# Kernel tuning notes

Measured on AMD Instinct MI355X. Metric: run time of the kernel, lower is better.

The kernel has to match this reference:

```python
import jax, jax.numpy as jnp
import numpy as np
import math

DIM = 1024
HEADS = 16
B, N = 2, 2048

POLY = jnp.array([-0.037, 0.481, -2.3, 4.917, -1.791], dtype=jnp.float32)


def adaptive_temperature_softmax(logits):
    # logits: [b, h, n, n]
    original_probs = jax.nn.softmax(logits, axis=-1)
    entropy = jnp.sum(-original_probs * jnp.log(original_probs + 1e-9), axis=-1, keepdims=True)
    e2 = entropy * entropy
    poly_result = POLY[0] * e2 * e2 + POLY[1] * e2 * entropy + POLY[2] * e2 + POLY[3] * entropy + POLY[4]
    beta = jnp.where(entropy > 0.5, jnp.maximum(poly_result, 1.0), 1.0)
    return jax.nn.softmax(logits * beta, axis=-1)


def setup_inputs() -> dict:
    key = jax.random.key(0)
    ks = jax.random.split(key, 5)
    s = 1.0 / math.sqrt(DIM)
    return {
        "x": jax.random.normal(ks[0], (B, N, DIM), dtype=jnp.float32),
        "Wq": jax.random.normal(ks[1], (DIM, DIM), dtype=jnp.float32) * s,
        "Wk": jax.random.normal(ks[2], (DIM, DIM), dtype=jnp.float32) * s,
        "Wv": jax.random.normal(ks[3], (DIM, DIM), dtype=jnp.float32) * s,
        "Wo": jax.random.normal(ks[4], (DIM, DIM), dtype=jnp.float32) * s,
        "bo": jnp.zeros((DIM,), dtype=jnp.float32),
    }


def reference(x, Wq, Wk, Wv, Wo, bo):
    b, n, d = x.shape
    h = HEADS
    hd = d // h
    # torch nn.Linear: y = x @ W.T (+ bias)
    def proj(W):
        t = x @ W.T  # [b, n, d]
        return t.reshape(b, n, h, hd).transpose(0, 2, 1, 3)  # [b, h, n, hd]
    q, k, v = proj(Wq), proj(Wk), proj(Wv)
    sim = jnp.einsum('bhid,bhjd->bhij', q, k) / math.sqrt(hd)
    neg = -jnp.finfo(sim.dtype).max
    causal = jnp.triu(jnp.ones((n, n), dtype=bool), k=1)  # True above diagonal
    sim = jnp.where(causal, neg, sim)
    attn = adaptive_temperature_softmax(sim)
    out = jnp.einsum('bhij,bhjd->bhid', attn, v)
    out = out.transpose(0, 2, 1, 3).reshape(b, n, d)
    return out @ Wo.T + bo
```

## Files before the change

### kernel.cpp

```cpp
#include <hip/hip_runtime.h>
#include <math.h>

#define B_   2
#define N_   2048
#define D_   1024
#define H_   16
#define HD_  64
#define BH_  32
#define M_   4096

typedef __bf16 bf16x8 __attribute__((ext_vector_type(8)));
typedef float  f32x4  __attribute__((ext_vector_type(4)));

__device__ inline unsigned short f2b(float f) {
    unsigned u = __float_as_uint(f);
    u += 0x7FFFu + ((u >> 16) & 1u);
    return (unsigned short)(u >> 16);
}
__device__ inline unsigned short f2b_fast(float f) {
    return (unsigned short)((__float_as_uint(f) + 0x8000u) >> 16);
}

__global__ __launch_bounds__(256)
void cvt_all(const float* __restrict__ x,  const float* __restrict__ wq,
             const float* __restrict__ wk, const float* __restrict__ wv,
             const float* __restrict__ wo, ushort* __restrict__ dst)
{
    int i = blockIdx.x * 256 + threadIdx.x;
    if (i >= 2097152) return;
    int fi = i * 4;
    const float* s; int off;
    if (fi < 4194304) { s = x; off = fi; }
    else {
        int r = fi - 4194304;
        int wsel = r >> 20;
        off = r & 1048575;
        s = (wsel == 0) ? wq : (wsel == 1) ? wk : (wsel == 2) ? wv : wo;
    }
    float4 f = *(const float4*)(s + off);
    ushort4 o;
    o.x = f2b(f.x); o.y = f2b(f.y); o.z = f2b(f.z); o.w = f2b(f.w);
    *(ushort4*)(dst + fi) = o;
}

__global__ __launch_bounds__(256)
void gemm_qkv(const ushort* __restrict__ A,
              const ushort* __restrict__ W0, const ushort* __restrict__ W1,
              const ushort* __restrict__ W2,
              ushort* __restrict__ O0, ushort* __restrict__ O1,
              ushort* __restrict__ O2)
{
    const int z = blockIdx.z;
    const ushort* W = (z == 0) ? W0 : (z == 1) ? W1 : W2;

    __shared__ alignas(16) ushort As[128][40];
    __shared__ alignas(16) ushort Bs[128][40];

    const int t = threadIdx.x;
    const int lane = t & 63, w = t >> 6;
    const int quad = lane >> 4, l15 = lane & 15;
    const int wm = (w >> 1) * 64, wn = (w & 1) * 64;
    const int tileM = blockIdx.x * 128, tileN = blockIdx.y * 128;

    const int r0 = t >> 2, r1 = 64 + (t >> 2);
    const int cg = (t & 3) * 8;
    const ushort* GA0 = A + (size_t)(tileM + r0) * D_ + cg;
    const ushort* GA1 = A + (size_t)(tileM + r1) * D_ + cg;
    const ushort* GB0 = W + (size_t)(tileN + r0) * D_ + cg;
    const ushort* GB1 = W + (size_t)(tileN + r1) * D_ + cg;

    f32x4 acc[4][4];
#pragma unroll
    for (int mt = 0; mt < 4; ++mt)
#pragma unroll
        for (int nt = 0; nt < 4; ++nt) acc[mt][nt] = (f32x4){0.f, 0.f, 0.f, 0.f};

    uint4 pa0 = *(const uint4*)GA0, pa1 = *(const uint4*)GA1;
    uint4 pb0 = *(const uint4*)GB0, pb1 = *(const uint4*)GB1;

    for (int k0 = 0; k0 < D_; k0 += 32) {
        __syncthreads();
        *(uint4*)&As[r0][cg] = pa0;
        *(uint4*)&As[r1][cg] = pa1;
        *(uint4*)&Bs[r0][cg] = pb0;
        *(uint4*)&Bs[r1][cg] = pb1;
        __syncthreads();
        if (k0 + 32 < D_) {
            pa0 = *(const uint4*)(GA0 + k0 + 32);
            pa1 = *(const uint4*)(GA1 + k0 + 32);
            pb0 = *(const uint4*)(GB0 + k0 + 32);
            pb1 = *(const uint4*)(GB1 + k0 + 32);
        }

        bf16x8 af[4], bf[4];
#pragma unroll
        for (int mt = 0; mt < 4; ++mt) af[mt] = *(const bf16x8*)&As[wm + mt * 16 + l15][quad * 8];
#pragma unroll
        for (int nt = 0; nt < 4; ++nt) bf[nt] = *(const bf16x8*)&Bs[wn + nt * 16 + l15][quad * 8];
#pragma unroll
        for (int mt = 0; mt < 4; ++mt)
#pragma unroll
            for (int nt = 0; nt < 4; ++nt)
                acc[mt][nt] = __builtin_amdgcn_mfma_f32_16x16x32_bf16(af[mt], bf[nt], acc[mt][nt], 0, 0, 0);
    }

    ushort* O = (z == 0) ? O0 : (z == 1) ? O1 : O2;
    const float scl = (z == 0) ? 0.18033688f : 1.0f;
#pragma unroll
    for (int mt = 0; mt < 4; ++mt)
#pragma unroll
        for (int nt = 0; nt < 4; ++nt) {
            if (z == 2) {
                int rg0 = tileM + wm + mt * 16 + quad * 4;
                int cgc = tileN + wn + nt * 16 + l15;
                int b = rg0 >> 11, n0 = rg0 & (N_ - 1);
                int h = cgc >> 6, dd = cgc & 63;
                ushort4 o4;
                o4.x = f2b(acc[mt][nt][0]); o4.y = f2b(acc[mt][nt][1]);
                o4.z = f2b(acc[mt][nt][2]); o4.w = f2b(acc[mt][nt][3]);
                *(ushort4*)&O[((size_t)((b * H_ + h) * HD_ + dd)) * N_ + n0] = o4;
            } else {
#pragma unroll
                for (int r = 0; r < 4; ++r) {
                    int rg = tileM + wm + mt * 16 + quad * 4 + r;
                    int cgc = tileN + wn + nt * 16 + l15;
                    int b = rg >> 11, n = rg & (N_ - 1);
                    int h = cgc >> 6, dd = cgc & 63;
                    O[(((size_t)(b * H_ + h)) * N_ + n) * HD_ + dd] = f2b(acc[mt][nt][r] * scl);
                }
            }
        }
}

__global__ __launch_bounds__(256)
void gemm_fin(const ushort* __restrict__ A, const ushort* __restrict__ W,
              const float* __restrict__ bias, float* __restrict__ Of)
{
    __shared__ alignas(16) ushort As[128][40];
    __shared__ alignas(16) ushort Bs[64][40];

    const int t = threadIdx.x;
    const int lane = t & 63, w = t >> 6;
    const int quad = lane >> 4, l15 = lane & 15;
    const int wm = (w >> 1) * 64, wn = (w & 1) * 32;
    const int tileM = blockIdx.x * 128, tileN = blockIdx.y * 64;

    const int r0 = t >> 2, r1 = 64 + (t >> 2);
    const int cg = (t & 3) * 8;
    const ushort* GA0 = A + (size_t)(tileM + r0) * D_ + cg;
    const ushort* GA1 = A + (size_t)(tileM + r1) * D_ + cg;
    const ushort* GB0 = W + (size_t)(tileN + r0) * D_ + cg;

    f32x4 acc[4][2];
#pragma unroll
    for (int mt = 0; mt < 4; ++mt)
#pragma unroll
        for (int nt = 0; nt < 2; ++nt) acc[mt][nt] = (f32x4){0.f, 0.f, 0.f, 0.f};

    uint4 pa0 = *(const uint4*)GA0, pa1 = *(const uint4*)GA1;
    uint4 pb0 = *(const uint4*)GB0;

    for (int k0 = 0; k0 < D_; k0 += 32) {
        __syncthreads();
        *(uint4*)&As[r0][cg] = pa0;
        *(uint4*)&As[r1][cg] = pa1;
        *(uint4*)&Bs[r0 & 63][cg] = pb0;
        __syncthreads();
        if (k0 + 32 < D_) {
            pa0 = *(const uint4*)(GA0 + k0 + 32);
            pa1 = *(const uint4*)(GA1 + k0 + 32);
            pb0 = *(const uint4*)(GB0 + k0 + 32);
        }

        bf16x8 af[4], bf[2];
#pragma unroll
        for (int mt = 0; mt < 4; ++mt) af[mt] = *(const bf16x8*)&As[wm + mt * 16 + l15][quad * 8];
#pragma unroll
        for (int nt = 0; nt < 2; ++nt) bf[nt] = *(const bf16x8*)&Bs[wn + nt * 16 + l15][quad * 8];
#pragma unroll
        for (int mt = 0; mt < 4; ++mt)
#pragma unroll
            for (int nt = 0; nt < 2; ++nt)
                acc[mt][nt] = __builtin_amdgcn_mfma_f32_16x16x32_bf16(af[mt], bf[nt], acc[mt][nt], 0, 0, 0);
    }

#pragma unroll
    for (int mt = 0; mt < 4; ++mt)
#pragma unroll
        for (int nt = 0; nt < 2; ++nt)
#pragma unroll
            for (int r = 0; r < 4; ++r) {
                int rg = tileM + wm + mt * 16 + quad * 4 + r;
                int cgc = tileN + wn + nt * 16 + l15;
                Of[(size_t)rg * D_ + cgc] = acc[mt][nt][r] + bias[cgc];
            }
}

__global__ __launch_bounds__(256)
void attn_mfma(const ushort* __restrict__ Q, const ushort* __restrict__ K,
               const ushort* __restrict__ VT, ushort* __restrict__ AO)
{
    const int bid = blockIdx.x;
    const int qt = 31 - (bid >> 5);
    const int bh = bid & 31;
    const size_t kvbase = (size_t)bh * N_ * HD_;

    __shared__ alignas(16) ushort Ks[128][72];
    __shared__ alignas(16) ushort Vs[64][136];
    __shared__ alignas(16) ushort Ps[4][4][296];

    const int t = threadIdx.x;
    const int lane = t & 63, w = t >> 6;
    const int quad = lane >> 4, l15 = lane & 15;
    const float SH2 = 11.5416913f;
    const float LN2 = 0.69314718f;

    const int skey = t >> 3;
    const int skc  = (t & 7) * 8;
    const ushort* KS = K + kvbase + (size_t)skey * HD_ + skc;
    const int vhd = t >> 4;
    const int vkc = (t & 15) * 8;
    const ushort* VS = VT + kvbase + (size_t)vhd * N_ + vkc;

    const int qrow = w * 16 + quad * 4;
    const int qglob = qt * 64 + qrow;
    const int b = bh >> 4, h = bh & 15;
    const int nCh = (qt + 2) >> 1;

    bf16x8 aq0, aq1;
    {
        const size_t qr = kvbase + (size_t)(qt * 64 + w * 16 + l15) * HD_;
        aq0 = *(const bf16x8*)&Q[qr + quad * 8];
        aq1 = *(const bf16x8*)&Q[qr + 32 + quad * 8];
    }

    float ez[4] = {0.f, 0.f, 0.f, 0.f};
    float sz[4] = {0.f, 0.f, 0.f, 0.f};

    uint4 k0 = *(const uint4*)KS;
    uint4 k1 = *(const uint4*)(KS + 32 * HD_);
    uint4 k2 = *(const uint4*)(KS + 64 * HD_);
    uint4 k3 = *(const uint4*)(KS + 96 * HD_);
    for (int c = 0; c < nCh; ++c) {
        __syncthreads();
        *(uint4*)&Ks[skey][skc]      = k0;
        *(uint4*)&Ks[32 + skey][skc] = k1;
        *(uint4*)&Ks[64 + skey][skc] = k2;
        *(uint4*)&Ks[96 + skey][skc] = k3;
        __syncthreads();
        if (c + 1 < nCh) {
            const ushort* nb = KS + (size_t)(c + 1) * (128 * HD_);
            k0 = *(const uint4*)nb;
            k1 = *(const uint4*)(nb + 32 * HD_);
            k2 = *(const uint4*)(nb + 64 * HD_);
            k3 = *(const uint4*)(nb + 96 * HD_);
        }
        if (c + 1 < nCh) {
#pragma unroll
            for (int nt = 0; nt < 8; ++nt) {
                f32x4 sv = (f32x4){0.f, 0.f, 0.f, 0.f};
                sv = __builtin_amdgcn_mfma_f32_16x16x32_bf16(aq0, *(const bf16x8*)&Ks[nt * 16 + l15][quad * 8], sv, 0, 0, 0);
                sv = __builtin_amdgcn_mfma_f32_16x16x32_bf16(aq1, *(const bf16x8*)&Ks[nt * 16 + l15][32 + quad * 8], sv, 0, 0, 0);
#pragma unroll
                for (int r = 0; r < 4; ++r) {
                    float sh = sv[r] - SH2;
                    float e = __builtin_amdgcn_exp2f(sh);
                    ez[r] += e;
                    sz[r] = fmaf(e, sh, sz[r]);
                }
            }
        } else {
            const int tiles = (((qt + 1) * 64) - c * 128) >> 4;
            const int kb0 = c * 128;
            for (int nt = 0; nt < tiles; ++nt) {
                f32x4 sv = (f32x4){0.f, 0.f, 0.f, 0.f};
                sv = __builtin_amdgcn_mfma_f32_16x16x32_bf16(aq0, *(const bf16x8*)&Ks[nt * 16 + l15][quad * 8], sv, 0, 0, 0);
                sv = __builtin_amdgcn_mfma_f32_16x16x32_bf16(aq1, *(const bf16x8*)&Ks[nt * 16 + l15][32 + quad * 8], sv, 0, 0, 0);
                const int kcol = kb0 + nt * 16 + l15;
#pragma unroll
                for (int r = 0; r < 4; ++r) {
                    float sh = sv[r] - SH2;
                    float e = (kcol <= qglob + r) ? __builtin_amdgcn_exp2f(sh) : 0.f;
                    ez[r] += e;
                    sz[r] = fmaf(e, sh, sz[r]);
                }
            }
        }
    }
#pragma unroll
    for (int r = 0; r < 4; ++r) {
#pragma unroll
        for (int off = 1; off < 16; off <<= 1) {
            ez[r] += __shfl_xor(ez[r], off);
            sz[r] += __shfl_xor(sz[r], off);
        }
    }

    float nbs[4], bl[4];
#pragma unroll
    for (int r = 0; r < 4; ++r) {
        float Z = ez[r];
        float Hh = LN2 * (__builtin_amdgcn_logf(Z) - sz[r] / Z);
        float bb = 1.f;
        if (Hh > 0.5f) {
            float e2 = Hh * Hh;
            float pp = -0.037f * e2 * e2 + 0.481f * e2 * Hh - 2.3f * e2 + 4.917f * Hh - 1.791f;
            bb = fmaxf(pp, 1.f);
        }
        bl[r] = bb;
        nbs[r] = -bb * SH2;
    }

    f32x4 ov[4];
#pragma unroll
    for (int nt = 0; nt < 4; ++nt) ov[nt] = (f32x4){0.f, 0.f, 0.f, 0.f};
    float zp[4] = {0.f, 0.f, 0.f, 0.f};

    k0 = *(const uint4*)KS;
    k1 = *(const uint4*)(KS + 32 * HD_);
    k2 = *(const uint4*)(KS + 64 * HD_);
    k3 = *(const uint4*)(KS + 96 * HD_);
    uint4 v0 = *(const uint4*)VS;
    uint4 v1 = *(const uint4*)(VS + 16 * N_);
    uint4 v2 = *(const uint4*)(VS + 32 * N_);
    uint4 v3 = *(const uint4*)(VS + 48 * N_);
    for (int c = 0; c < nCh; ++c) {
        __syncthreads();
        *(uint4*)&Ks[skey][skc]      = k0;
        *(uint4*)&Ks[32 + skey][skc] = k1;
        *(uint4*)&Ks[64 + skey][skc] = k2;
        *(uint4*)&Ks[96 + skey][skc] = k3;
        *(uint4*)&Vs[vhd][vkc]       = v0;
        *(uint4*)&Vs[16 + vhd][vkc]  = v1;
        *(uint4*)&Vs[32 + vhd][vkc]  = v2;
        *(uint4*)&Vs[48 + vhd][vkc]  = v3;
        __syncthreads();
        if (c + 1 < nCh) {
            const ushort* nk = KS + (size_t)(c + 1) * (128 * HD_);
            k0 = *(const uint4*)nk;
            k1 = *(const uint4*)(nk + 32 * HD_);
            k2 = *(const uint4*)(nk + 64 * HD_);
            k3 = *(const uint4*)(nk + 96 * HD_);
            const ushort* nv = VS + (c + 1) * 128;
            v0 = *(const uint4*)nv;
            v1 = *(const uint4*)(nv + 16 * N_);
            v2 = *(const uint4*)(nv + 32 * N_);
            v3 = *(const uint4*)(nv + 48 * N_);
        }
        const int halves = min(2, (qt + 1) - c * 2);
        for (int hh = 0; hh < halves; ++hh) {
            const bool diag = (c * 2 + hh == qt);

            float wv[4][4];
#pragma unroll
            for (int nt = 0; nt < 4; ++nt) {
                f32x4 sv = (f32x4){0.f, 0.f, 0.f, 0.f};
                sv = __builtin_amdgcn_mfma_f32_16x16x32_bf16(aq0, *(const bf16x8*)&Ks[hh * 64 + nt * 16 + l15][quad * 8], sv, 0, 0, 0);
                sv = __builtin_amdgcn_mfma_f32_16x16x32_bf16(aq1, *(const bf16x8*)&Ks[hh * 64 + nt * 16 + l15][32 + quad * 8], sv, 0, 0, 0);
                const int kcol = nt * 16 + l15;
#pragma unroll
                for (int r = 0; r < 4; ++r) {
                    float e = __builtin_amdgcn_exp2f(fmaf(bl[r], sv[r], nbs[r]));
                    wv[nt][r] = (!diag || (kcol <= qrow + r)) ? e : 0.f;
                }
            }
#pragma unroll
            for (int nt = 0; nt < 4; ++nt)
#pragma unroll
                for (int r = 0; r < 4; ++r)
                    Ps[w][quad][r * 72 + nt * 16 + l15] = f2b_fast(wv[nt][r]);
#pragma unroll
            for (int r = 0; r < 4; ++r)
                zp[r] += (wv[0][r] + wv[1][r]) + (wv[2][r] + wv[3][r]);

            bf16x8 pa0 = *(const bf16x8*)&Ps[w][l15 >> 2][(l15 & 3) * 72 + quad * 8];
            bf16x8 pa1 = *(const bf16x8*)&Ps[w][l15 >> 2][(l15 & 3) * 72 + 32 + quad * 8];
#pragma unroll
            for (int nt = 0; nt < 4; ++nt) {
                ov[nt] = __builtin_amdgcn_mfma_f32_16x16x32_bf16(pa0, *(const bf16x8*)&Vs[nt * 16 + l15][hh * 64 + quad * 8], ov[nt], 0, 0, 0);
                ov[nt] = __builtin_amdgcn_mfma_f32_16x16x32_bf16(pa1, *(const bf16x8*)&Vs[nt * 16 + l15][hh * 64 + 32 + quad * 8], ov[nt], 0, 0, 0);
            }
        }
    }
#pragma unroll
    for (int r = 0; r < 4; ++r)
#pragma unroll
        for (int off = 1; off < 16; off <<= 1) zp[r] += __shfl_xor(zp[r], off);

#pragma unroll
    for (int r = 0; r < 4; ++r) {
        int qg = qt * 64 + w * 16 + quad * 4 + r;
        float inv = 1.f / zp[r];
        size_t rowoff = ((size_t)(b * N_ + qg)) * D_ + h * HD_;
#pragma unroll
        for (int nt = 0; nt < 4; ++nt)
            AO[rowoff + nt * 16 + l15] = f2b(ov[nt][r] * inv);
    }
}

extern "C" void kernel_launch(void* const* d_in, const int* in_sizes, int n_in,
                              void* d_out, int out_size, void* d_ws, size_t ws_size,
                              hipStream_t stream)
{
    const float* x  = (const float*)d_in[0];
    const float* Wq = (const float*)d_in[1];
    const float* Wk = (const float*)d_in[2];
    const float* Wv = (const float*)d_in[3];
    const float* Wo = (const float*)d_in[4];
    const float* bo = (const float*)d_in[5];
    float* out = (float*)d_out;

    ushort* ws  = (ushort*)d_ws;
    ushort* xb  = ws;
    ushort* wqb = ws + 4194304;
    ushort* wkb = ws + 5242880;
    ushort* wvb = ws + 6291456;
    ushort* wob = ws + 7340032;
    ushort* Qb  = ws + 8388608;
    ushort* Kb  = ws + 12582912;
    ushort* Vtb = ws + 16777216;
    ushort* aob = ws + 20971520;

    cvt_all<<<8192, 256, 0, stream>>>(x, Wq, Wk, Wv, Wo, xb);

    gemm_qkv<<<dim3(32, 8, 3), 256, 0, stream>>>(
        xb, wqb, wkb, wvb, Qb, Kb, Vtb);

    attn_mfma<<<dim3(1024), 256, 0, stream>>>(Qb, Kb, Vtb, aob);

    gemm_fin<<<dim3(32, 16), 256, 0, stream>>>(aob, wob, bo, out);
}
```

Baseline: 202.2 us.

## Process two 64-row query tiles per attention block to reuse K/V loads

Each attention block now handles a 128-row query tile as two 64-row sub-tiles (A and B) that share every K and V chunk loaded into shared memory, and the grid is halved to 512 blocks. The aim is to halve global and shared-memory traffic for K/V and amortise the barriers over twice the MFMA work. The cost is more registers per thread (two sets of Q fragments, accumulators and statistics), which may lower occupancy. Fewer, heavier blocks may also leave compute units less evenly loaded under the causal work imbalance.

```diff
diff --git a/kernel.cpp b/kernel.cpp
--- a/kernel.cpp
+++ b/kernel.cpp
@@ -201,7 +201,7 @@
                const ushort* __restrict__ VT, ushort* __restrict__ AO)
 {
     const int bid = blockIdx.x;
-    const int qt = 31 - (bid >> 5);
+    const int qtt = 15 - (bid >> 5);
     const int bh = bid & 31;
     const size_t kvbase = (size_t)bh * N_ * HD_;
 
@@ -222,20 +222,21 @@
     const int vkc = (t & 15) * 8;
     const ushort* VS = VT + kvbase + (size_t)vhd * N_ + vkc;
 
-    const int qrow = w * 16 + quad * 4;
-    const int qglob = qt * 64 + qrow;
+    const int qrowL = w * 16 + quad * 4;
     const int b = bh >> 4, h = bh & 15;
-    const int nCh = (qt + 2) >> 1;
-
-    bf16x8 aq0, aq1;
+    const int nCh = qtt + 1;
+
+    bf16x8 aq0A, aq1A, aq0B, aq1B;
     {
-        const size_t qr = kvbase + (size_t)(qt * 64 + w * 16 + l15) * HD_;
-        aq0 = *(const bf16x8*)&Q[qr + quad * 8];
-        aq1 = *(const bf16x8*)&Q[qr + 32 + quad * 8];
-    }
-
-    float ez[4] = {0.f, 0.f, 0.f, 0.f};
-    float sz[4] = {0.f, 0.f, 0.f, 0.f};
+        const size_t qrA = kvbase + (size_t)(qtt * 128 + w * 16 + l15) * HD_;
+        aq0A = *(const bf16x8*)&Q[qrA + quad * 8];
+        aq1A = *(const bf16x8*)&Q[qrA + 32 + quad * 8];
+        aq0B = *(const bf16x8*)&Q[qrA + 64 * HD_ + quad * 8];
+        aq1B = *(const bf16x8*)&Q[qrA + 64 * HD_ + 32 + quad * 8];
+    }
+
+    float ezA[4] = {0.f, 0.f, 0.f, 0.f}, szA[4] = {0.f, 0.f, 0.f, 0.f};
+    float ezB[4] = {0.f, 0.f, 0.f, 0.f}, szB[4] = {0.f, 0.f, 0.f, 0.f};
 
     uint4 k0 = *(const uint4*)KS;
     uint4 k1 = *(const uint4*)(KS + 32 * HD_);
@@ -255,34 +256,60 @@
             k2 = *(const uint4*)(nb + 64 * HD_);
             k3 = *(const uint4*)(nb + 96 * HD_);
         }
-        if (c + 1 < nCh) {
+        if (c < qtt) {
 #pragma unroll
             for (int nt = 0; nt < 8; ++nt) {
-                f32x4 sv = (f32x4){0.f, 0.f, 0.f, 0.f};
-                sv = __builtin_amdgcn_mfma_f32_16x16x32_bf16(aq0, *(const bf16x8*)&Ks[nt * 16 + l15][quad * 8], sv, 0, 0, 0);
-                sv = __builtin_amdgcn_mfma_f32_16x16x32_bf16(aq1, *(const bf16x8*)&Ks[nt * 16 + l15][32 + quad * 8], sv, 0, 0, 0);
+                bf16x8 kf0 = *(const bf16x8*)&Ks[nt * 16 + l15][quad * 8];
+                bf16x8 kf1 = *(const bf16x8*)&Ks[nt * 16 + l15][32 + quad * 8];
+                f32x4 svA = (f32x4){0.f, 0.f, 0.f, 0.f};
+                svA = __builtin_amdgcn_mfma_f32_16x16x32_bf16(aq0A, kf0, svA, 0, 0, 0);
+                svA = __builtin_amdgcn_mfma_f32_16x16x32_bf16(aq1A, kf1, svA, 0, 0, 0);
+                f32x4 svB = (f32x4){0.f, 0.f, 0.f, 0.f};
+                svB = __builtin_amdgcn_mfma_f32_16x16x32_bf16(aq0B, kf0, svB, 0, 0, 0);
+                svB = __builtin_amdgcn_mfma_f32_16x16x32_bf16(aq1B, kf1, svB, 0, 0, 0);
 #pragma unroll
                 for (int r = 0; r < 4; ++r) {
-                    float sh = sv[r] - SH2;
-                    float e = __builtin_amdgcn_exp2f(sh);
-                    ez[r] += e;
-                    sz[r] = fmaf(e, sh, sz[r]);
+                    float shA = svA[r] - SH2, shB = svB[r] - SH2;
+                    float eA = __builtin_amdgcn_exp2f(shA);
+                    float eB = __builtin_amdgcn_exp2f(shB);
+                    ezA[r] += eA; szA[r] = fmaf(eA, shA, szA[r]);
+                    ezB[r] += eB; szB[r] = fmaf(eB, shB, szB[r]);
                 }
             }
         } else {
-            const int tiles = (((qt + 1) * 64) - c * 128) >> 4;
-            const int kb0 = c * 128;
-            for (int nt = 0; nt < tiles; ++nt) {
-                f32x4 sv = (f32x4){0.f, 0.f, 0.f, 0.f};
-                sv = __builtin_amdgcn_mfma_f32_16x16x32_bf16(aq0, *(const bf16x8*)&Ks[nt * 16 + l15][quad * 8], sv, 0, 0, 0);
-                sv = __builtin_amdgcn_mfma_f32_16x16x32_bf16(aq1, *(const bf16x8*)&Ks[nt * 16 + l15][32 + quad * 8], sv, 0, 0, 0);
-                const int kcol = kb0 + nt * 16 + l15;
+#pragma unroll
+            for (int nt = 0; nt < 4; ++nt) {
+                bf16x8 kf0 = *(const bf16x8*)&Ks[nt * 16 + l15][quad * 8];
+                bf16x8 kf1 = *(const bf16x8*)&Ks[nt * 16 + l15][32 + quad * 8];
+                f32x4 svA = (f32x4){0.f, 0.f, 0.f, 0.f};
+                svA = __builtin_amdgcn_mfma_f32_16x16x32_bf16(aq0A, kf0, svA, 0, 0, 0);
+                svA = __builtin_amdgcn_mfma_f32_16x16x32_bf16(aq1A, kf1, svA, 0, 0, 0);
+                f32x4 svB = (f32x4){0.f, 0.f, 0.f, 0.f};
+                svB = __builtin_amdgcn_mfma_f32_16x16x32_bf16(aq0B, kf0, svB, 0, 0, 0);
+                svB = __builtin_amdgcn_mfma_f32_16x16x32_bf16(aq1B, kf1, svB, 0, 0, 0);
+                const int kcol = nt * 16 + l15;
 #pragma unroll
                 for (int r = 0; r < 4; ++r) {
-                    float sh = sv[r] - SH2;
-                    float e = (kcol <= qglob + r) ? __builtin_amdgcn_exp2f(sh) : 0.f;
-                    ez[r] += e;
-                    sz[r] = fmaf(e, sh, sz[r]);
+                    float shA = svA[r] - SH2, shB = svB[r] - SH2;
+                    float eA = (kcol <= qrowL + r) ? __builtin_amdgcn_exp2f(shA) : 0.f;
+                    float eB = __builtin_amdgcn_exp2f(shB);
+                    ezA[r] += eA; szA[r] = fmaf(eA, shA, szA[r]);
+                    ezB[r] += eB; szB[r] = fmaf(eB, shB, szB[r]);
+                }
+            }
+#pragma unroll
+            for (int nt = 4; nt < 8; ++nt) {
+                bf16x8 kf0 = *(const bf16x8*)&Ks[nt * 16 + l15][quad * 8];
+                bf16x8 kf1 = *(const bf16x8*)&Ks[nt * 16 + l15][32 + quad * 8];
+                f32x4 svB = (f32x4){0.f, 0.f, 0.f, 0.f};
+                svB = __builtin_amdgcn_mfma_f32_16x16x32_bf16(aq0B, kf0, svB, 0, 0, 0);
+                svB = __builtin_amdgcn_mfma_f32_16x16x32_bf16(aq1B, kf1, svB, 0, 0, 0);
+                const int kcol = (nt - 4) * 16 + l15;
+#pragma unroll
+                for (int r = 0; r < 4; ++r) {
+                    float shB = svB[r] - SH2;
+                    float eB = (kcol <= qrowL + r) ? __builtin_amdgcn_exp2f(shB) : 0.f;
+                    ezB[r] += eB; szB[r] = fmaf(eB, shB, szB[r]);
                 }
             }
         }
@@ -291,30 +318,43 @@
     for (int r = 0; r < 4; ++r) {
 #pragma unroll
         for (int off = 1; off < 16; off <<= 1) {
-            ez[r] += __shfl_xor(ez[r], off);
-            sz[r] += __shfl_xor(sz[r], off);
-        }
-    }
-
-    float nbs[4], bl[4];
+            ezA[r] += __shfl_xor(ezA[r], off);
+            szA[r] += __shfl_xor(szA[r], off);
+            ezB[r] += __shfl_xor(ezB[r], off);
+            szB[r] += __shfl_xor(szB[r], off);
+        }
+    }
+
+    float nbsA[4], blA[4], nbsB[4], blB[4];
 #pragma unroll
     for (int r = 0; r < 4; ++r) {
-        float Z = ez[r];
-        float Hh = LN2 * (__builtin_amdgcn_logf(Z) - sz[r] / Z);
+        float Z = ezA[r];
+        float Hh = LN2 * (__builtin_amdgcn_logf(Z) - szA[r] / Z);
         float bb = 1.f;
         if (Hh > 0.5f) {
             float e2 = Hh * Hh;
             float pp = -0.037f * e2 * e2 + 0.481f * e2 * Hh - 2.3f * e2 + 4.917f * Hh - 1.791f;
             bb = fmaxf(pp, 1.f);
         }
-        bl[r] = bb;
-        nbs[r] = -bb * SH2;
-    }
-
-    f32x4 ov[4];
-#pragma unroll
-    for (int nt = 0; nt < 4; ++nt) ov[nt] = (f32x4){0.f, 0.f, 0.f, 0.f};
-    float zp[4] = {0.f, 0.f, 0.f, 0.f};
+        blA[r] = bb; nbsA[r] = -bb * SH2;
+        Z = ezB[r];
+        Hh = LN2 * (__builtin_amdgcn_logf(Z) - szB[r] / Z);
+        bb = 1.f;
+        if (Hh > 0.5f) {
+            float e2 = Hh * Hh;
+            float pp = -0.037f * e2 * e2 + 0.481f * e2 * Hh - 2.3f * e2 + 4.917f * Hh - 1.791f;
+            bb = fmaxf(pp, 1.f);
+        }
+        blB[r] = bb; nbsB[r] = -bb * SH2;
+    }
+
+    f32x4 ovA[4], ovB[4];
+#pragma unroll
+    for (int nt = 0; nt < 4; ++nt) {
+        ovA[nt] = (f32x4){0.f, 0.f, 0.f, 0.f};
+        ovB[nt] = (f32x4){0.f, 0.f, 0.f, 0.f};
+    }
+    float zpA[4] = {0.f, 0.f, 0.f, 0.f}, zpB[4] = {0.f, 0.f, 0.f, 0.f};
 
     k0 = *(const uint4*)KS;
     k1 = *(const uint4*)(KS + 32 * HD_);
@@ -347,54 +387,97 @@
             v2 = *(const uint4*)(nv + 32 * N_);
             v3 = *(const uint4*)(nv + 48 * N_);
         }
-        const int halves = min(2, (qt + 1) - c * 2);
-        for (int hh = 0; hh < halves; ++hh) {
-            const bool diag = (c * 2 + hh == qt);
-
-            float wv[4][4];
-#pragma unroll
-            for (int nt = 0; nt < 4; ++nt) {
-                f32x4 sv = (f32x4){0.f, 0.f, 0.f, 0.f};
-                sv = __builtin_amdgcn_mfma_f32_16x16x32_bf16(aq0, *(const bf16x8*)&Ks[hh * 64 + nt * 16 + l15][quad * 8], sv, 0, 0, 0);
-                sv = __builtin_amdgcn_mfma_f32_16x16x32_bf16(aq1, *(const bf16x8*)&Ks[hh * 64 + nt * 16 + l15][32 + quad * 8], sv, 0, 0, 0);
-                const int kcol = nt * 16 + l15;
-#pragma unroll
-                for (int r = 0; r < 4; ++r) {
-                    float e = __builtin_amdgcn_exp2f(fmaf(bl[r], sv[r], nbs[r]));
-                    wv[nt][r] = (!diag || (kcol <= qrow + r)) ? e : 0.f;
-                }
-            }
-#pragma unroll
-            for (int nt = 0; nt < 4; ++nt)
+#pragma unroll
+        for (int hh = 0; hh < 2; ++hh) {
+            const bool diagA = (c == qtt && hh == 0);
+            const bool skipA = (c == qtt && hh == 1);
+            const bool diagB = (c == qtt && hh == 1);
+
+            if (!skipA) {
+                float wv[4][4];
+#pragma unroll
+                for (int nt = 0; nt < 4; ++nt) {
+                    f32x4 sv = (f32x4){0.f, 0.f, 0.f, 0.f};
+                    sv = __builtin_amdgcn_mfma_f32_16x16x32_bf16(aq0A, *(const bf16x8*)&Ks[hh * 64 + nt * 16 + l15][quad * 8], sv, 0, 0, 0);
+                    sv = __builtin_amdgcn_mfma_f32_16x16x32_bf16(aq1A, *(const bf16x8*)&Ks[hh * 64 + nt * 16 + l15][32 + quad * 8], sv, 0, 0, 0);
+                    const int kcol = nt * 16 + l15;
+#pragma unroll
+                    for (int r = 0; r < 4; ++r) {
+                        float e = __builtin_amdgcn_exp2f(fmaf(blA[r], sv[r], nbsA[r]));
+                        wv[nt][r] = (!diagA || (kcol <= qrowL + r)) ? e : 0.f;
+                    }
+                }
+#pragma unroll
+                for (int nt = 0; nt < 4; ++nt)
+#pragma unroll
+                    for (int r = 0; r < 4; ++r)
+                        Ps[w][quad][r * 72 + nt * 16 + l15] = f2b_fast(wv[nt][r]);
 #pragma unroll
                 for (int r = 0; r < 4; ++r)
-                    Ps[w][quad][r * 72 + nt * 16 + l15] = f2b_fast(wv[nt][r]);
-#pragma unroll
-            for (int r = 0; r < 4; ++r)
-                zp[r] += (wv[0][r] + wv[1][r]) + (wv[2][r] + wv[3][r]);
-
-            bf16x8 pa0 = *(const bf16x8*)&Ps[w][l15 >> 2][(l15 & 3) * 72 + quad * 8];
-            bf16x8 pa1 = *(const bf16x8*)&Ps[w][l15 >> 2][(l15 & 3) * 72 + 32 + quad * 8];
-#pragma unroll
-            for (int nt = 0; nt < 4; ++nt) {
-                ov[nt] = __builtin_amdgcn_mfma_f32_16x16x32_bf16(pa0, *(const bf16x8*)&Vs[nt * 16 + l15][hh * 64 + quad * 8], ov[nt], 0, 0, 0);
-                ov[nt] = __builtin_amdgcn_mfma_f32_16x16x32_bf16(pa1, *(const bf16x8*)&Vs[nt * 16 + l15][hh * 64 + 32 + quad * 8], ov[nt], 0, 0, 0);
+                    zpA[r] += (wv[0][r] + wv[1][r]) + (wv[2][r] + wv[3][r]);
+
+                bf16x8 pa0 = *(const bf16x8*)&Ps[w][l15 >> 2][(l15 & 3) * 72 + quad * 8];
+                bf16x8 pa1 = *(const bf16x8*)&Ps[w][l15 >> 2][(l15 & 3) * 72 + 32 + quad * 8];
+#pragma unroll
+                for (int nt = 0; nt < 4; ++nt) {
+                    ovA[nt] = __builtin_amdgcn_mfma_f32_16x16x32_bf16(pa0, *(const bf16x8*)&Vs[nt * 16 + l15][hh * 64 + quad * 8], ovA[nt], 0, 0, 0);
+                    ovA[nt] = __builtin_amdgcn_mfma_f32_16x16x32_bf16(pa1, *(const bf16x8*)&Vs[nt * 16 + l15][hh * 64 + 32 + quad * 8], ovA[nt], 0, 0, 0);
+                }
+            }
+
+            {
+                float wv[4][4];
+#pragma unroll
+                for (int nt = 0; nt < 4; ++nt) {
+                    f32x4 sv = (f32x4){0.f, 0.f, 0.f, 0.f};
+                    sv = __builtin_amdgcn_mfma_f32_16x16x32_bf16(aq0B, *(const bf16x8*)&Ks[hh * 64 + nt * 16 + l15][quad * 8], sv, 0, 0, 0);
+                    sv = __builtin_amdgcn_mfma_f32_16x16x32_bf16(aq1B, *(const bf16x8*)&Ks[hh * 64 + nt * 16 + l15][32 + quad * 8], sv, 0, 0, 0);
+                    const int kcol = nt * 16 + l15;
+#pragma unroll
+                    for (int r = 0; r < 4; ++r) {
+                        float e = __builtin_amdgcn_exp2f(fmaf(blB[r], sv[r], nbsB[r]));
+                        wv[nt][r] = (!diagB || (kcol <= qrowL + r)) ? e : 0.f;
+                    }
+                }
+#pragma unroll
+                for (int nt = 0; nt < 4; ++nt)
+#pragma unroll
+                    for (int r = 0; r < 4; ++r)
+                        Ps[w][quad][r * 72 + nt * 16 + l15] = f2b_fast(wv[nt][r]);
+#pragma unroll
+                for (int r = 0; r < 4; ++r)
+                    zpB[r] += (wv[0][r] + wv[1][r]) + (wv[2][r] + wv[3][r]);
+
+                bf16x8 pa0 = *(const bf16x8*)&Ps[w][l15 >> 2][(l15 & 3) * 72 + quad * 8];
+                bf16x8 pa1 = *(const bf16x8*)&Ps[w][l15 >> 2][(l15 & 3) * 72 + 32 + quad * 8];
+#pragma unroll
+                for (int nt = 0; nt < 4; ++nt) {
+                    ovB[nt] = __builtin_amdgcn_mfma_f32_16x16x32_bf16(pa0, *(const bf16x8*)&Vs[nt * 16 + l15][hh * 64 + quad * 8], ovB[nt], 0, 0, 0);
+                    ovB[nt] = __builtin_amdgcn_mfma_f32_16x16x32_bf16(pa1, *(const bf16x8*)&Vs[nt * 16 + l15][hh * 64 + 32 + quad * 8], ovB[nt], 0, 0, 0);
+                }
             }
         }
     }
 #pragma unroll
     for (int r = 0; r < 4; ++r)
 #pragma unroll
-        for (int off = 1; off < 16; off <<= 1) zp[r] += __shfl_xor(zp[r], off);
+        for (int off = 1; off < 16; off <<= 1) {
+            zpA[r] += __shfl_xor(zpA[r], off);
+            zpB[r] += __shfl_xor(zpB[r], off);
+        }
 
 #pragma unroll
     for (int r = 0; r < 4; ++r) {
-        int qg = qt * 64 + w * 16 + quad * 4 + r;
-        float inv = 1.f / zp[r];
-        size_t rowoff = ((size_t)(b * N_ + qg)) * D_ + h * HD_;
-#pragma unroll
-        for (int nt = 0; nt < 4; ++nt)
-            AO[rowoff + nt * 16 + l15] = f2b(ov[nt][r] * inv);
+        int qgA = qtt * 128 + w * 16 + quad * 4 + r;
+        float invA = 1.f / zpA[r];
+        float invB = 1.f / zpB[r];
+        size_t roA = ((size_t)(b * N_ + qgA)) * D_ + h * HD_;
+        size_t roB = ((size_t)(b * N_ + qgA + 64)) * D_ + h * HD_;
+#pragma unroll
+        for (int nt = 0; nt < 4; ++nt) {
+            AO[roA + nt * 16 + l15] = f2b(ovA[nt][r] * invA);
+            AO[roB + nt * 16 + l15] = f2b(ovB[nt][r] * invB);
+        }
     }
 }
 
@@ -426,7 +509,7 @@
     gemm_qkv<<<dim3(32, 8, 3), 256, 0, stream>>>(
         xb, wqb, wkb, wvb, Qb, Kb, Vtb);
 
-    attn_mfma<<<dim3(1024), 256, 0, stream>>>(Qb, Kb, Vtb, aob);
+    attn_mfma<<<dim3(512), 256, 0, stream>>>(Qb, Kb, Vtb, aob);
 
     gemm_fin<<<dim3(32, 16), 256, 0, stream>>>(aob, wob, bo, out);
 }
```

Result: slower. 213.4 us (+5.6%).
